# Kernel tuning notes

Hardware: AMD Instinct MI355X
Metric: run time of the kernel (lower is better)

Reference implementation:

```python
import jax, jax.numpy as jnp
import numpy as np

N, F, E = 65536, 64, 16   # batch, fields, embedding_size
H1, H2 = 8, 4             # hidden_dims
BN_EPS = 1e-5


def setup_inputs() -> dict:
    key = jax.random.key(0)
    ks = jax.random.split(key, 12)
    rn = lambda k, shape, sc=1.0: jax.random.normal(k, shape, dtype=jnp.float32) * sc
    return {
        "Xa": rn(ks[0], (N, F)),
        "Xc": rn(ks[1], (N, F)),
        # per-field Linear(1,1) weights/biases (two first-order embedding lists)
        "w1": rn(ks[2], (F,)), "b1": rn(ks[3], (F,)),
        "w2": rn(ks[4], (F,)), "b2": rn(ks[5], (F,)),
        # per-field Linear(1,E) weights/biases (two second-order embedding lists)
        "W1": rn(ks[6], (F, E)), "B1": rn(ks[7], (F, E)),
        "W2": rn(ks[8], (F, E)), "B2": rn(ks[9], (F, E)),
        # deep MLP: linear_1 (F*E -> 8) + BN, linear_2 (8 -> 4). No final layer (init bug).
        "lin1_w": rn(ks[10], (H1, F * E), 0.01), "lin1_b": jnp.zeros((H1,), jnp.float32),
        "bn1_gamma": jnp.ones((H1,), jnp.float32), "bn1_beta": jnp.zeros((H1,), jnp.float32),
        "lin2_w": rn(ks[11], (H2, H1), 0.01), "lin2_b": jnp.full((H2,), 0.21, jnp.float32),
    }


def reference(Xa, Xc, w1, b1, w2, b2, W1, B1, W2, B2,
              lin1_w, lin1_b, bn1_gamma, bn1_beta, lin2_w, lin2_b):
    n = Xa.shape[0]
    # ---- FM first order (faithful to the torch broadcast: arr_2[i] is (N,N)
    # with entry [r,c] = Xa[r,i]*(w2[i]*Xc[c,i]+b2[i]); only mean over the
    # concat dim is consumed, so compute the column-mean analytically). ----
    first1 = (w1 * Xa + b1) * Xc                         # (N,F)
    xc_mean = jnp.mean(Xc, axis=0)                       # (F,)
    first2_cmean = Xa * (w2 * xc_mean + b2)              # (N,F) = mean over c of arr_2
    fm_first_mean = jnp.mean(first1 + first2_cmean, axis=1, keepdims=True)  # (N,1)

    # ---- FM second order: per-field (N,E) embeddings, fully batched. ----
    Xa3 = Xa[:, :, None]                                 # (N,F,1)
    Xc3 = Xc[:, :, None]
    emb = (Xa3 * W1 + B1) * Xc3 + Xa3 * (W2 * Xc3 + B2)  # (N,F,E)
    s = emb.sum(axis=1)                                  # (N,E)
    fm_second = 0.5 * (s * s - (emb * emb).sum(axis=1))  # (N,E)
    fm_second_mean = jnp.mean(fm_second, axis=1, keepdims=True)  # (N,1)

    # ---- deep part: cat of per-field (N,E) -> (N, F*E), field-major. ----
    deep = emb.reshape(n, F * E)
    h = deep @ lin1_w.T + lin1_b                         # (N,8)
    mu = h.mean(axis=0)
    var = h.var(axis=0)                                  # biased, as BN training mode
    h = (h - mu) / jnp.sqrt(var + BN_EPS) * bn1_gamma + bn1_beta
    h = jnp.tanh(h)                                      # dropout = identity (eval)
    h = h @ lin2_w.T + lin2_b                            # (N,4) — no final projection (init bug)
    deep_mean = h.mean(axis=1, keepdims=True)            # (N,1)

    return fm_first_mean + fm_second_mean + deep_mean    # (N,1)
```

## Files before the change

### kernel.cpp

```cpp
#include <hip/hip_runtime.h>
#include <math.h>

#define NROWS 65536
#define BN_EPS 1e-5f

#define OFF_PARTIAL 0
#define OFF_H       65536
#define OFF_REC     589824
#define OFF_BLKT    595200
#define OFF_T       677120

__global__ __launch_bounds__(64) void precompute_kernel(
    const float* __restrict__ W1, const float* __restrict__ B1,
    const float* __restrict__ W2, const float* __restrict__ B2,
    const float* __restrict__ lin1_w, const float* __restrict__ w1,
    const float* __restrict__ b1, const float* __restrict__ b2,
    float* __restrict__ rec)
{
    int f = blockIdx.x, t = threadIdx.x;
    __shared__ float u[16], x[16], y[16];
    if (t < 16) {
        float uu = W1[f * 16 + t] + W2[f * 16 + t];
        float xx = B1[f * 16 + t];
        float yy = B2[f * 16 + t];
        u[t] = uu; x[t] = xx; y[t] = yy;
        rec[f * 84 + t]      = uu;
        rec[f * 84 + 16 + t] = xx;
        rec[f * 84 + 32 + t] = yy;
    }
    __syncthreads();
    if (t < 24) {
        int j = t & 7, which = t >> 3;
        const float* src = (which == 0) ? u : (which == 1) ? x : y;
        const float* lw = lin1_w + j * 1024 + f * 16;
        float acc = 0.f;
#pragma unroll
        for (int e = 0; e < 16; e++) acc = fmaf(src[e], lw[e], acc);
        rec[f * 84 + 48 + which * 8 + j] = acc;
    } else if (t < 30) {
        int q = t - 24;
        const float* s1 = (q == 0 || q == 3 || q == 4) ? u : (q == 1 || q == 5) ? x : y;
        const float* s2 = (q == 0) ? u : (q == 1 || q == 3) ? x : y;
        float acc = 0.f;
#pragma unroll
        for (int e = 0; e < 16; e++) acc = fmaf(s1[e], s2[e], acc);
        rec[f * 84 + 72 + q] = (q < 3 ? 1.f : 2.f) * acc;
    } else if (t == 30) {
        rec[f * 84 + 78] = w1[f];
        rec[f * 84 + 79] = b1[f];
        rec[f * 84 + 80] = b2[f];
        rec[f * 84 + 81] = 0.f;
        rec[f * 84 + 82] = 0.f;
        rec[f * 84 + 83] = 0.f;
    }
}

__global__ __launch_bounds__(256, 3) void main_kernel(
    const float* __restrict__ Xa, const float* __restrict__ Xc,
    const float* __restrict__ rec, const float* __restrict__ lin1_b,
    float* __restrict__ ws_partial, float* __restrict__ ws_h,
    float* __restrict__ ws_blkT)
{
    __shared__ float cmb[4][64][29];

    int tid  = threadIdx.x;
    int lane = tid & 63;
    int wv   = tid >> 6;
    int wu   = __builtin_amdgcn_readfirstlane(wv);
    int blk  = blockIdx.x;
    int row  = blk * 64 + lane;
    int f0   = wu * 16;

    const float4* pa = (const float4*)(Xa + (size_t)row * 64 + f0);
    const float4* pc = (const float4*)(Xc + (size_t)row * 64 + f0);
    float a_[16], c_[16];
#pragma unroll
    for (int k = 0; k < 4; k++) {
        float4 av = pa[k], cv = pc[k];
        a_[k * 4] = av.x; a_[k * 4 + 1] = av.y; a_[k * 4 + 2] = av.z; a_[k * 4 + 3] = av.w;
        c_[k * 4] = cv.x; c_[k * 4 + 1] = cv.y; c_[k * 4 + 2] = cv.z; c_[k * 4 + 3] = cv.w;
    }

    float s[16], hh[8];
#pragma unroll
    for (int e = 0; e < 16; e++) s[e] = 0.f;
#pragma unroll
    for (int j = 0; j < 8; j++) hh[j] = 0.f;
    float p1 = 0.f, p2a = 0.f, qsum = 0.f;

    const float* recw = rec + (size_t)f0 * 84;
#pragma unroll
    for (int i = 0; i < 16; i++) {
        const float* r = recw + i * 84;
        float a = a_[i], c = c_[i];
        float pp = a * c;
        p1  = fmaf(fmaf(r[78], a, r[79]), c, p1);
        p2a = fmaf(a, r[80], p2a);
        qsum = fmaf(pp * pp, r[72], qsum);
        qsum = fmaf(c * c,   r[73], qsum);
        qsum = fmaf(a * a,   r[74], qsum);
        qsum = fmaf(pp * c,  r[75], qsum);
        qsum = fmaf(pp * a,  r[76], qsum);
        qsum = fmaf(pp,      r[77], qsum);
#pragma unroll
        for (int e = 0; e < 16; e++)
            s[e] = fmaf(pp, r[e], fmaf(c, r[16 + e], fmaf(a, r[32 + e], s[e])));
#pragma unroll
        for (int j = 0; j < 8; j++)
            hh[j] = fmaf(pp, r[48 + j], fmaf(c, r[56 + j], fmaf(a, r[64 + j], hh[j])));
    }

    {
        float cs[16];
#pragma unroll
        for (int i = 0; i < 16; i++) cs[i] = c_[i];
#pragma unroll
        for (int off = 1; off < 64; off <<= 1) {
#pragma unroll
            for (int i = 0; i < 16; i++) cs[i] += __shfl_xor(cs[i], off);
        }
        if (lane == 0) {
#pragma unroll
            for (int i = 0; i < 16; i++)
                ws_blkT[(size_t)(f0 + i) * 1024 + blk] = cs[i];
        }
    }

#pragma unroll
    for (int e = 0; e < 16; e++) cmb[wv][lane][e] = s[e];
#pragma unroll
    for (int j = 0; j < 8; j++) cmb[wv][lane][16 + j] = hh[j];
    cmb[wv][lane][24] = p1;
    cmb[wv][lane][25] = p2a;
    cmb[wv][lane][26] = qsum;
    __syncthreads();

    if (tid < 64) {
        float S[16], H[8], P1 = 0.f, P2 = 0.f, Q = 0.f;
#pragma unroll
        for (int e = 0; e < 16; e++) S[e] = 0.f;
#pragma unroll
        for (int j = 0; j < 8; j++) H[j] = 0.f;
#pragma unroll
        for (int w = 0; w < 4; w++) {
#pragma unroll
            for (int e = 0; e < 16; e++) S[e] += cmb[w][tid][e];
#pragma unroll
            for (int j = 0; j < 8; j++) H[j] += cmb[w][tid][16 + j];
            P1 += cmb[w][tid][24];
            P2 += cmb[w][tid][25];
            Q  += cmb[w][tid][26];
        }
#pragma unroll
        for (int j = 0; j < 8; j++) H[j] += lin1_b[j];

        float ss = 0.f;
#pragma unroll
        for (int e = 0; e < 16; e++) ss = fmaf(S[e], S[e], ss);
        float fm2 = (ss - Q) * (0.5f / 16.f);
        int rr = blk * 64 + tid;
        ws_partial[rr] = (P1 + P2) * (1.f / 64.f) + fm2;
        *(float4*)(ws_h + (size_t)rr * 8)     = make_float4(H[0], H[1], H[2], H[3]);
        *(float4*)(ws_h + (size_t)rr * 8 + 4) = make_float4(H[4], H[5], H[6], H[7]);

        float v[16];
#pragma unroll
        for (int j = 0; j < 8; j++) { v[j] = H[j]; v[8 + j] = H[j] * H[j]; }
#pragma unroll
        for (int off = 1; off < 64; off <<= 1) {
#pragma unroll
            for (int i = 0; i < 16; i++) v[i] += __shfl_xor(v[i], off);
        }
        if (tid == 0) {
#pragma unroll
            for (int i = 0; i < 16; i++)
                ws_blkT[(size_t)(64 + i) * 1024 + blk] = v[i];
        }
    }
}

__global__ __launch_bounds__(256) void reduce_kernel(
    const float* __restrict__ ws_blkT, float* __restrict__ T)
{
    int gtid = blockIdx.x * 256 + threadIdx.x;
    int v = gtid >> 6;
    int lane = gtid & 63;
    const float* p = ws_blkT + (size_t)v * 1024 + lane;
    float acc = 0.f;
#pragma unroll
    for (int k = 0; k < 16; k++) acc += p[k * 64];
#pragma unroll
    for (int off = 32; off; off >>= 1) acc += __shfl_xor(acc, off);
    if (lane == 0) T[v] = acc;
}

__global__ __launch_bounds__(256) void final_kernel(
    const float* __restrict__ Xa, const float* __restrict__ w2,
    const float* __restrict__ gamma, const float* __restrict__ beta,
    const float* __restrict__ lin2_w, const float* __restrict__ lin2_b,
    const float* __restrict__ T, const float* __restrict__ ws_partial,
    const float* __restrict__ ws_h, float* __restrict__ out)
{
    __shared__ float sg[64], sScale[8], sShift[8], sColw[8];
    __shared__ float sBsum;
    int tid = threadIdx.x;
    if (tid < 64) {
        sg[tid] = w2[tid] * (T[tid] * (1.f / 65536.f));
    } else if (tid < 72) {
        int j = tid - 64;
        float mu  = T[64 + j] * (1.f / 65536.f);
        float var = T[72 + j] * (1.f / 65536.f) - mu * mu;
        float sc = gamma[j] / sqrtf(var + BN_EPS);
        sScale[j] = sc;
        sShift[j] = beta[j] - mu * sc;
    } else if (tid < 80) {
        int j = tid - 72;
        sColw[j] = lin2_w[j] + lin2_w[8 + j] + lin2_w[16 + j] + lin2_w[24 + j];
    } else if (tid == 80) {
        sBsum = lin2_b[0] + lin2_b[1] + lin2_b[2] + lin2_b[3];
    }
    __syncthreads();

    int row  = (blockIdx.x * 256 + tid) >> 1;
    int half = tid & 1;
    int fo   = half * 32;

    const float4* xa4 = (const float4*)(Xa + (size_t)row * 64 + fo);
    float p2b = 0.f;
#pragma unroll
    for (int k = 0; k < 8; k++) {
        float4 vv = xa4[k];
        int b = fo + k * 4;
        p2b += vv.x * sg[b] + vv.y * sg[b + 1] + vv.z * sg[b + 2] + vv.w * sg[b + 3];
    }

    float4 hq = *(const float4*)(ws_h + (size_t)row * 8 + half * 4);
    float hv[4] = {hq.x, hq.y, hq.z, hq.w};
    float dmp = 0.f;
#pragma unroll
    for (int jj = 0; jj < 4; jj++) {
        int j = half * 4 + jj;
        float hn = tanhf(hv[jj] * sScale[j] + sShift[j]);
        dmp = fmaf(hn, sColw[j], dmp);
    }

    float val = p2b * (1.f / 64.f) + dmp * 0.25f;
    val += __shfl_xor(val, 1);
    if (!half)
        out[row] = val + ws_partial[row] + sBsum * 0.25f;
}

extern "C" void kernel_launch(void* const* d_in, const int* in_sizes, int n_in,
                              void* d_out, int out_size, void* d_ws, size_t ws_size,
                              hipStream_t stream) {
    const float* Xa        = (const float*)d_in[0];
    const float* Xc        = (const float*)d_in[1];
    const float* w1        = (const float*)d_in[2];
    const float* b1        = (const float*)d_in[3];
    const float* w2        = (const float*)d_in[4];
    const float* b2        = (const float*)d_in[5];
    const float* W1        = (const float*)d_in[6];
    const float* B1        = (const float*)d_in[7];
    const float* W2        = (const float*)d_in[8];
    const float* B2        = (const float*)d_in[9];
    const float* lin1_w    = (const float*)d_in[10];
    const float* lin1_b    = (const float*)d_in[11];
    const float* bn1_gamma = (const float*)d_in[12];
    const float* bn1_beta  = (const float*)d_in[13];
    const float* lin2_w    = (const float*)d_in[14];
    const float* lin2_b    = (const float*)d_in[15];

    float* ws  = (float*)d_ws;
    float* out = (float*)d_out;

    float* ws_partial = ws + OFF_PARTIAL;
    float* ws_h       = ws + OFF_H;
    float* ws_rec     = ws + OFF_REC;
    float* ws_blkT    = ws + OFF_BLKT;
    float* ws_T       = ws + OFF_T;

    precompute_kernel<<<64, 64, 0, stream>>>(W1, B1, W2, B2, lin1_w,
                                             w1, b1, b2, ws_rec);
    main_kernel<<<1024, 256, 0, stream>>>(Xa, Xc, ws_rec, lin1_b,
                                          ws_partial, ws_h, ws_blkT);
    reduce_kernel<<<20, 256, 0, stream>>>(ws_blkT, ws_T);
    final_kernel<<<512, 256, 0, stream>>>(Xa, w2, bn1_gamma, bn1_beta,
                                          lin2_w, lin2_b, ws_T,
                                          ws_partial, ws_h, out);
}
```

Measured before the change: 147.3 us.

## Process two 64-row tiles per block and compute Xc column sums via coalesced loads

```diff
diff --git a/kernel.cpp b/kernel.cpp
--- a/kernel.cpp
+++ b/kernel.cpp
@@ -3,12 +3,13 @@
 
 #define NROWS 65536
 #define BN_EPS 1e-5f
+#define NBLK   512
 
 #define OFF_PARTIAL 0
 #define OFF_H       65536
 #define OFF_REC     589824
 #define OFF_BLKT    595200
-#define OFF_T       677120
+#define OFF_T       636160
 
 __global__ __launch_bounds__(64) void precompute_kernel(
     const float* __restrict__ W1, const float* __restrict__ B1,
@@ -55,126 +56,158 @@
     }
 }
 
-__global__ __launch_bounds__(256, 3) void main_kernel(
+__global__ __launch_bounds__(256, 4) void main_kernel(
     const float* __restrict__ Xa, const float* __restrict__ Xc,
     const float* __restrict__ rec, const float* __restrict__ lin1_b,
     float* __restrict__ ws_partial, float* __restrict__ ws_h,
     float* __restrict__ ws_blkT)
 {
     __shared__ float cmb[4][64][29];
+    __shared__ float scol[256];
 
     int tid  = threadIdx.x;
     int lane = tid & 63;
     int wv   = tid >> 6;
     int wu   = __builtin_amdgcn_readfirstlane(wv);
     int blk  = blockIdx.x;
-    int row  = blk * 64 + lane;
     int f0   = wu * 16;
-
-    const float4* pa = (const float4*)(Xa + (size_t)row * 64 + f0);
-    const float4* pc = (const float4*)(Xc + (size_t)row * 64 + f0);
-    float a_[16], c_[16];
+    int rowbase = blk * 128;
+
+    {
+        int col = tid & 63, grp = tid >> 6;
+        float acc = 0.f;
+        for (int r = grp; r < 128; r += 4)
+            acc += Xc[(size_t)(rowbase + r) * 64 + col];
+        scol[tid] = acc;
+    }
+    __syncthreads();
+    if (tid < 64) {
+        float t = scol[tid] + scol[64 + tid] + scol[128 + tid] + scol[192 + tid];
+        ws_blkT[(size_t)tid * NBLK + blk] = t;
+    }
+
+    size_t rb0 = ((size_t)rowbase + lane) * 64 + f0;
+    const float4* pa0 = (const float4*)(Xa + rb0);
+    const float4* pc0 = (const float4*)(Xc + rb0);
+    const float4* pa1 = (const float4*)(Xa + rb0 + 64 * 64);
+    const float4* pc1 = (const float4*)(Xc + rb0 + 64 * 64);
+
+    float s0[16], s1[16], h0[8], h1[8];
+#pragma unroll
+    for (int e = 0; e < 16; e++) { s0[e] = 0.f; s1[e] = 0.f; }
+#pragma unroll
+    for (int j = 0; j < 8; j++) { h0[j] = 0.f; h1[j] = 0.f; }
+    float p1a = 0.f, p1b = 0.f, p2a0 = 0.f, p2a1 = 0.f, q0 = 0.f, q1 = 0.f;
+
+    const float* recw = rec + (size_t)f0 * 84;
 #pragma unroll
     for (int k = 0; k < 4; k++) {
-        float4 av = pa[k], cv = pc[k];
-        a_[k * 4] = av.x; a_[k * 4 + 1] = av.y; a_[k * 4 + 2] = av.z; a_[k * 4 + 3] = av.w;
-        c_[k * 4] = cv.x; c_[k * 4 + 1] = cv.y; c_[k * 4 + 2] = cv.z; c_[k * 4 + 3] = cv.w;
-    }
-
-    float s[16], hh[8];
-#pragma unroll
-    for (int e = 0; e < 16; e++) s[e] = 0.f;
-#pragma unroll
-    for (int j = 0; j < 8; j++) hh[j] = 0.f;
-    float p1 = 0.f, p2a = 0.f, qsum = 0.f;
-
-    const float* recw = rec + (size_t)f0 * 84;
-#pragma unroll
-    for (int i = 0; i < 16; i++) {
-        const float* r = recw + i * 84;
-        float a = a_[i], c = c_[i];
-        float pp = a * c;
-        p1  = fmaf(fmaf(r[78], a, r[79]), c, p1);
-        p2a = fmaf(a, r[80], p2a);
-        qsum = fmaf(pp * pp, r[72], qsum);
-        qsum = fmaf(c * c,   r[73], qsum);
-        qsum = fmaf(a * a,   r[74], qsum);
-        qsum = fmaf(pp * c,  r[75], qsum);
-        qsum = fmaf(pp * a,  r[76], qsum);
-        qsum = fmaf(pp,      r[77], qsum);
-#pragma unroll
-        for (int e = 0; e < 16; e++)
-            s[e] = fmaf(pp, r[e], fmaf(c, r[16 + e], fmaf(a, r[32 + e], s[e])));
-#pragma unroll
-        for (int j = 0; j < 8; j++)
-            hh[j] = fmaf(pp, r[48 + j], fmaf(c, r[56 + j], fmaf(a, r[64 + j], hh[j])));
-    }
-
-    {
-        float cs[16];
-#pragma unroll
-        for (int i = 0; i < 16; i++) cs[i] = c_[i];
+        float4 A0 = pa0[k], C0 = pc0[k];
+        float4 A1 = pa1[k], C1 = pc1[k];
+        float av0[4] = {A0.x, A0.y, A0.z, A0.w};
+        float cv0[4] = {C0.x, C0.y, C0.z, C0.w};
+        float av1[4] = {A1.x, A1.y, A1.z, A1.w};
+        float cv1[4] = {C1.x, C1.y, C1.z, C1.w};
+#pragma unroll
+        for (int uu = 0; uu < 4; uu++) {
+            const float* r = recw + (k * 4 + uu) * 84;
+            {
+                float a = av0[uu], c = cv0[uu], pp = a * c;
+                p1a  = fmaf(fmaf(r[78], a, r[79]), c, p1a);
+                p2a0 = fmaf(a, r[80], p2a0);
+                q0 = fmaf(pp * pp, r[72], q0);
+                q0 = fmaf(c * c,   r[73], q0);
+                q0 = fmaf(a * a,   r[74], q0);
+                q0 = fmaf(pp * c,  r[75], q0);
+                q0 = fmaf(pp * a,  r[76], q0);
+                q0 = fmaf(pp,      r[77], q0);
+#pragma unroll
+                for (int e = 0; e < 16; e++)
+                    s0[e] = fmaf(pp, r[e], fmaf(c, r[16+e], fmaf(a, r[32+e], s0[e])));
+#pragma unroll
+                for (int j = 0; j < 8; j++)
+                    h0[j] = fmaf(pp, r[48+j], fmaf(c, r[56+j], fmaf(a, r[64+j], h0[j])));
+            }
+            {
+                float a = av1[uu], c = cv1[uu], pp = a * c;
+                p1b  = fmaf(fmaf(r[78], a, r[79]), c, p1b);
+                p2a1 = fmaf(a, r[80], p2a1);
+                q1 = fmaf(pp * pp, r[72], q1);
+                q1 = fmaf(c * c,   r[73], q1);
+                q1 = fmaf(a * a,   r[74], q1);
+                q1 = fmaf(pp * c,  r[75], q1);
+                q1 = fmaf(pp * a,  r[76], q1);
+                q1 = fmaf(pp,      r[77], q1);
+#pragma unroll
+                for (int e = 0; e < 16; e++)
+                    s1[e] = fmaf(pp, r[e], fmaf(c, r[16+e], fmaf(a, r[32+e], s1[e])));
+#pragma unroll
+                for (int j = 0; j < 8; j++)
+                    h1[j] = fmaf(pp, r[48+j], fmaf(c, r[56+j], fmaf(a, r[64+j], h1[j])));
+            }
+        }
+    }
+
+    float bn[16];
+#pragma unroll
+    for (int i = 0; i < 16; i++) bn[i] = 0.f;
+
+#pragma unroll
+    for (int g = 0; g < 2; g++) {
+        __syncthreads();
+#pragma unroll
+        for (int e = 0; e < 16; e++) cmb[wv][lane][e] = g ? s1[e] : s0[e];
+#pragma unroll
+        for (int j = 0; j < 8; j++) cmb[wv][lane][16 + j] = g ? h1[j] : h0[j];
+        cmb[wv][lane][24] = g ? p1b : p1a;
+        cmb[wv][lane][25] = g ? p2a1 : p2a0;
+        cmb[wv][lane][26] = g ? q1 : q0;
+        __syncthreads();
+
+        if (tid < 64) {
+            float S[16], H[8], P1 = 0.f, P2 = 0.f, Q = 0.f;
+#pragma unroll
+            for (int e = 0; e < 16; e++) S[e] = 0.f;
+#pragma unroll
+            for (int j = 0; j < 8; j++) H[j] = 0.f;
+#pragma unroll
+            for (int w = 0; w < 4; w++) {
+#pragma unroll
+                for (int e = 0; e < 16; e++) S[e] += cmb[w][tid][e];
+#pragma unroll
+                for (int j = 0; j < 8; j++) H[j] += cmb[w][tid][16 + j];
+                P1 += cmb[w][tid][24];
+                P2 += cmb[w][tid][25];
+                Q  += cmb[w][tid][26];
+            }
+#pragma unroll
+            for (int j = 0; j < 8; j++) H[j] += lin1_b[j];
+
+            float ss = 0.f;
+#pragma unroll
+            for (int e = 0; e < 16; e++) ss = fmaf(S[e], S[e], ss);
+            int rr = rowbase + g * 64 + tid;
+            ws_partial[rr] = (P1 + P2) * (1.f / 64.f) + (ss - Q) * (0.5f / 16.f);
+            *(float4*)(ws_h + (size_t)rr * 8)     = make_float4(H[0], H[1], H[2], H[3]);
+            *(float4*)(ws_h + (size_t)rr * 8 + 4) = make_float4(H[4], H[5], H[6], H[7]);
+#pragma unroll
+            for (int j = 0; j < 8; j++) {
+                bn[j]     += H[j];
+                bn[8 + j] += H[j] * H[j];
+            }
+        }
+    }
+
+    if (tid < 64) {
 #pragma unroll
         for (int off = 1; off < 64; off <<= 1) {
 #pragma unroll
-            for (int i = 0; i < 16; i++) cs[i] += __shfl_xor(cs[i], off);
-        }
-        if (lane == 0) {
-#pragma unroll
-            for (int i = 0; i < 16; i++)
-                ws_blkT[(size_t)(f0 + i) * 1024 + blk] = cs[i];
-        }
-    }
-
-#pragma unroll
-    for (int e = 0; e < 16; e++) cmb[wv][lane][e] = s[e];
-#pragma unroll
-    for (int j = 0; j < 8; j++) cmb[wv][lane][16 + j] = hh[j];
-    cmb[wv][lane][24] = p1;
-    cmb[wv][lane][25] = p2a;
-    cmb[wv][lane][26] = qsum;
-    __syncthreads();
-
-    if (tid < 64) {
-        float S[16], H[8], P1 = 0.f, P2 = 0.f, Q = 0.f;
-#pragma unroll
-        for (int e = 0; e < 16; e++) S[e] = 0.f;
-#pragma unroll
-        for (int j = 0; j < 8; j++) H[j] = 0.f;
-#pragma unroll
-        for (int w = 0; w < 4; w++) {
-#pragma unroll
-            for (int e = 0; e < 16; e++) S[e] += cmb[w][tid][e];
-#pragma unroll
-            for (int j = 0; j < 8; j++) H[j] += cmb[w][tid][16 + j];
-            P1 += cmb[w][tid][24];
-            P2 += cmb[w][tid][25];
-            Q  += cmb[w][tid][26];
-        }
-#pragma unroll
-        for (int j = 0; j < 8; j++) H[j] += lin1_b[j];
-
-        float ss = 0.f;
-#pragma unroll
-        for (int e = 0; e < 16; e++) ss = fmaf(S[e], S[e], ss);
-        float fm2 = (ss - Q) * (0.5f / 16.f);
-        int rr = blk * 64 + tid;
-        ws_partial[rr] = (P1 + P2) * (1.f / 64.f) + fm2;
-        *(float4*)(ws_h + (size_t)rr * 8)     = make_float4(H[0], H[1], H[2], H[3]);
-        *(float4*)(ws_h + (size_t)rr * 8 + 4) = make_float4(H[4], H[5], H[6], H[7]);
-
-        float v[16];
-#pragma unroll
-        for (int j = 0; j < 8; j++) { v[j] = H[j]; v[8 + j] = H[j] * H[j]; }
-#pragma unroll
-        for (int off = 1; off < 64; off <<= 1) {
-#pragma unroll
-            for (int i = 0; i < 16; i++) v[i] += __shfl_xor(v[i], off);
+            for (int i = 0; i < 16; i++) bn[i] += __shfl_xor(bn[i], off);
         }
         if (tid == 0) {
 #pragma unroll
             for (int i = 0; i < 16; i++)
-                ws_blkT[(size_t)(64 + i) * 1024 + blk] = v[i];
+                ws_blkT[(size_t)(64 + i) * NBLK + blk] = bn[i];
         }
     }
 }
@@ -185,10 +218,10 @@
     int gtid = blockIdx.x * 256 + threadIdx.x;
     int v = gtid >> 6;
     int lane = gtid & 63;
-    const float* p = ws_blkT + (size_t)v * 1024 + lane;
+    const float* p = ws_blkT + (size_t)v * NBLK + lane;
     float acc = 0.f;
 #pragma unroll
-    for (int k = 0; k < 16; k++) acc += p[k * 64];
+    for (int k = 0; k < 8; k++) acc += p[k * 64];
 #pragma unroll
     for (int off = 32; off; off >>= 1) acc += __shfl_xor(acc, off);
     if (lane == 0) T[v] = acc;
@@ -281,7 +314,7 @@
 
     precompute_kernel<<<64, 64, 0, stream>>>(W1, B1, W2, B2, lin1_w,
                                              w1, b1, b2, ws_rec);
-    main_kernel<<<1024, 256, 0, stream>>>(Xa, Xc, ws_rec, lin1_b,
+    main_kernel<<<NBLK, 256, 0, stream>>>(Xa, Xc, ws_rec, lin1_b,
                                           ws_partial, ws_h, ws_blkT);
     reduce_kernel<<<20, 256, 0, stream>>>(ws_blkT, ws_T);
     final_kernel<<<512, 256, 0, stream>>>(Xa, w2, bn1_gamma, bn1_beta,
```

New measurement: 129.2 us. 1.14x faster.
